# Optimization experiments

Measured on AMD Instinct MI355X. Metric: run time of the kernel, lower is better.

The kernel has to match this reference:

```python
import jax, jax.numpy as jnp
import numpy as np

N_HEAD = 16
D_K = 64


def _bn(x, g, b, eps=1e-5):
    # torch BatchNorm1d in training mode: biased batch variance
    m = jnp.mean(x, axis=0)
    v = jnp.var(x, axis=0)
    return (x - m) * jax.lax.rsqrt(v + eps) * g + b


def setup_inputs() -> dict:
    key = jax.random.key(0)
    ks = jax.random.split(key, 8)
    B, DX, NK, DKIN, H, DK, DO = 128, 1024, 1024, 512, N_HEAD, D_K, 512
    sc = 0.02
    return {
        "x": jax.random.normal(ks[0], (B, DX), dtype=jnp.float32),
        "k": jax.random.normal(ks[1], (B, NK, DKIN), dtype=jnp.float32),
        "bn1_g": jnp.ones((DX,), jnp.float32),
        "bn1_b": jnp.zeros((DX,), jnp.float32),
        "Wx": jax.random.normal(ks[2], (H * DK, DX), dtype=jnp.float32) * sc,
        "bx": jnp.zeros((H * DK,), jnp.float32),
        "Wk": jax.random.normal(ks[3], (H * DK, DKIN), dtype=jnp.float32) * sc,
        "bk": jnp.zeros((H * DK,), jnp.float32),
        "bn2_g": jnp.ones((DK,), jnp.float32),
        "bn2_b": jnp.zeros((DK,), jnp.float32),
        "Wlin": jax.random.normal(ks[4], (DK, DK), dtype=jnp.float32) * sc,
        "blin": jnp.zeros((DK,), jnp.float32),
        "Wo": jax.random.normal(ks[5], (DO, H * DK), dtype=jnp.float32) * sc,
        "bo": jnp.zeros((DO,), jnp.float32),
    }


def reference(x, k, bn1_g, bn1_b, Wx, bx, Wk, bk, bn2_g, bn2_b, Wlin, blin, Wo, bo):
    H, DK = N_HEAD, D_K
    B, DX = x.shape
    NK = k.shape[1]
    # outer BN + query projection (n_x == 1)
    xq = _bn(x, bn1_g, bn1_b) @ Wx.T + bx                     # (B, H*DK)
    xq = xq.reshape(B, H, DK).transpose(1, 0, 2).reshape(H * B, DK)
    kp = (k @ Wk.T + bk).reshape(B, NK, H, DK)
    kp = kp.transpose(2, 0, 1, 3).reshape(H * B, NK, DK)       # (H*B, NK, DK)
    # inner CrossAttention: BN + linear on the single query vector
    latent = _bn(xq, bn2_g, bn2_b) @ Wlin.T + blin             # (H*B, DK)
    u = jnp.einsum('bnd,bd->bn', kp, latent)                   # (H*B, NK)
    # softmax over the singleton query dim (dim=2) -> all ones, kept faithful
    attn = jax.nn.softmax(u[..., None], axis=-1)[..., 0]       # (H*B, NK)
    out = jnp.einsum('bnd,bn->bd', kp, attn)                   # (H*B, DK)
    out = out.reshape(H, B, DK).transpose(1, 0, 2).reshape(B, H * DK)
    x_hid = latent.reshape(H, B, DK).transpose(1, 0, 2).reshape(B, H * DK)
    # attn.view(n_head, batch, d_x_).permute(1,2,0).contiguous().view(batch, n_head, -1)
    attn_out = attn.reshape(H, B, NK).transpose(1, 2, 0).reshape(B, H, -1)
    return (attn_out, out @ Wo.T + bo, x_hid @ Wo.T + bo)
```

## Files before the change

### kernel.cpp

```cpp
#include <hip/hip_runtime.h>

typedef __attribute__((ext_vector_type(8))) short short8;
typedef __attribute__((ext_vector_type(4))) float floatx4;

__device__ __forceinline__ unsigned short f2bf(float f) {
    unsigned int x = __float_as_uint(f);
    x = x + 0x7FFFu + ((x >> 16) & 1u);
    return (unsigned short)(x >> 16);
}

__global__ __launch_bounds__(256) void k_reduce(
    const float* __restrict__ kk, float* __restrict__ part)
{
    int blk = blockIdx.x, tid = threadIdx.x;
    int b = blk >> 3, c = blk & 7;
    int f4 = tid & 127;
    int rh = tid >> 7;
    const float4* base = (const float4*)kk
        + ((size_t)(b * 1024 + c * 128 + rh) * 128 + f4);
    float4 acc = {0.f, 0.f, 0.f, 0.f};
    #pragma unroll 8
    for (int it = 0; it < 64; ++it) {
        float4 v = base[(size_t)it * 256];
        acc.x += v.x; acc.y += v.y; acc.z += v.z; acc.w += v.w;
    }
    __shared__ float red[2][512];
    red[rh][f4 * 4 + 0] = acc.x;
    red[rh][f4 * 4 + 1] = acc.y;
    red[rh][f4 * 4 + 2] = acc.z;
    red[rh][f4 * 4 + 3] = acc.w;
    __syncthreads();
    for (int j = tid; j < 512; j += 256)
        part[((size_t)(c * 128 + b) << 9) + j] = red[0][j] + red[1][j];
}

__global__ __launch_bounds__(256) void k_w2bf(
    const float* __restrict__ Wx, const float* __restrict__ Wk,
    const float* __restrict__ Wo, const float* __restrict__ Wl,
    unsigned short* __restrict__ Wxbf, unsigned short* __restrict__ Wkbf,
    unsigned short* __restrict__ Wobf, unsigned short* __restrict__ Wlbf)
{
    int f = blockIdx.x * 256 + threadIdx.x;
    const float* src; unsigned short* dst; int off;
    if (f < 262144)      { src = Wx; dst = Wxbf; off = f; }
    else if (f < 393216) { src = Wk; dst = Wkbf; off = f - 262144; }
    else if (f < 524288) { src = Wo; dst = Wobf; off = f - 393216; }
    else                 { src = Wl; dst = Wlbf; off = f - 524288; }
    float4 v = ((const float4*)src)[off];
    uint2 o;
    o.x = (unsigned int)f2bf(v.x) | ((unsigned int)f2bf(v.y) << 16);
    o.y = (unsigned int)f2bf(v.z) | ((unsigned int)f2bf(v.w) << 16);
    *(uint2*)(dst + off * 4) = o;
}

__global__ __launch_bounds__(256) void k_bn1_combine(
    const float* __restrict__ x, const float* __restrict__ g1,
    const float* __restrict__ b1, const float* __restrict__ part,
    unsigned short* __restrict__ xnbf, unsigned short* __restrict__ ksumbf)
{
    int blk = blockIdx.x, tid = threadIdx.x;
    if (blk < 4) {
        int c = blk * 256 + tid;
        float s = 0.f, ss = 0.f;
        #pragma unroll 8
        for (int b = 0; b < 128; ++b) {
            float v = x[b * 1024 + c];
            s += v; ss += v * v;
        }
        float m  = s * (1.f / 128.f);
        float va = ss * (1.f / 128.f) - m * m;
        float rs = rsqrtf(va + 1e-5f);
        float a  = rs * g1[c];
        float b2 = b1[c] - m * a;
        #pragma unroll 8
        for (int b = 0; b < 128; ++b)
            xnbf[b * 1024 + c] = f2bf(x[b * 1024 + c] * a + b2);
    } else {
        int idx = (blk - 4) * 256 + tid;
        int b = idx >> 6;
        int j0 = (idx & 63) * 8;
        float s[8];
        #pragma unroll
        for (int u = 0; u < 8; ++u) s[u] = 0.f;
        #pragma unroll
        for (int c = 0; c < 8; ++c) {
            const float4* p = (const float4*)(part + ((size_t)(c * 128 + b) << 9) + j0);
            float4 a0 = p[0], a1 = p[1];
            s[0] += a0.x; s[1] += a0.y; s[2] += a0.z; s[3] += a0.w;
            s[4] += a1.x; s[5] += a1.y; s[6] += a1.z; s[7] += a1.w;
        }
        uint4 v;
        v.x = (unsigned int)f2bf(s[0]) | ((unsigned int)f2bf(s[1]) << 16);
        v.y = (unsigned int)f2bf(s[2]) | ((unsigned int)f2bf(s[3]) << 16);
        v.z = (unsigned int)f2bf(s[4]) | ((unsigned int)f2bf(s[5]) << 16);
        v.w = (unsigned int)f2bf(s[6]) | ((unsigned int)f2bf(s[7]) << 16);
        *(uint4*)(ksumbf + b * 512 + j0) = v;
    }
}

template <typename OutT>
__global__ __launch_bounds__(256) void k_mfma(
    const unsigned short* __restrict__ A, int lda,
    const unsigned short* __restrict__ B, int ldb,
    const float* __restrict__ bias, float bscale,
    OutT* __restrict__ C, int ldc, int tilesN, int K)
{
    int gid = blockIdx.x * 256 + threadIdx.x;
    int wave = gid >> 6;
    int lane = threadIdx.x & 63;
    int tm = wave / tilesN, tn = wave % tilesN;
    int mn = lane & 15, q = lane >> 4;

    const short8* ap = (const short8*)(A + (size_t)(tm * 16 + mn) * lda + q * 8);
    const short8* bp = (const short8*)(B + (size_t)(tn * 16 + mn) * ldb + q * 8);

    floatx4 acc = {0.f, 0.f, 0.f, 0.f};
    #pragma unroll 4
    for (int k = 0; k < K; k += 32) {
        short8 a = *ap; ap += 4;
        short8 b = *bp; bp += 4;
        acc = __builtin_amdgcn_mfma_f32_16x16x32_bf16(a, b, acc, 0, 0, 0);
    }
    int col = tn * 16 + mn;
    float bv = bias[col] * bscale;
    #pragma unroll
    for (int r = 0; r < 4; ++r) {
        int row = tm * 16 + q * 4 + r;
        float v = acc[r] + bv;
        OutT* dst = C + (size_t)row * ldc + col;
        if constexpr (sizeof(OutT) == 2) *dst = (OutT)f2bf(v);
        else                             *dst = (OutT)v;
    }
}

__global__ __launch_bounds__(256) void k_bn2(
    const float* __restrict__ xq, const float* __restrict__ g2,
    const float* __restrict__ b2, float* __restrict__ ab)
{
    int d = blockIdx.x, tid = threadIdx.x;
    float s = 0.f, ss = 0.f;
    for (int e = tid; e < 2048; e += 256) {
        int b = e >> 4, h = e & 15;
        float v = xq[b * 1024 + h * 64 + d];
        s += v; ss += v * v;
    }
    __shared__ float r1[256], r2[256];
    r1[tid] = s; r2[tid] = ss;
    __syncthreads();
    for (int off = 128; off; off >>= 1) {
        if (tid < off) { r1[tid] += r1[tid + off]; r2[tid] += r2[tid + off]; }
        __syncthreads();
    }
    if (tid == 0) {
        float m  = r1[0] * (1.f / 2048.f);
        float va = r2[0] * (1.f / 2048.f) - m * m;
        float rs = rsqrtf(va + 1e-5f);
        float a  = rs * g2[d];
        ab[d] = a;
        ab[64 + d] = b2[d] - m * a;
    }
}

__global__ __launch_bounds__(256) void k_latent(
    const float* __restrict__ xq, const float* __restrict__ ab,
    const unsigned short* __restrict__ Wlbf, const float* __restrict__ bl,
    unsigned short* __restrict__ xhid)
{
    int tid = threadIdx.x;
    int r = tid >> 6, dp = tid & 63;
    int row = blockIdx.x * 4 + r;
    int h = row >> 7, b = row & 127;
    __shared__ float xs[4][64];
    xs[r][dp] = xq[b * 1024 + h * 64 + dp] * ab[dp] + ab[64 + dp];
    __syncthreads();
    float dot = bl[dp];
    #pragma unroll 16
    for (int d = 0; d < 64; ++d)
        dot += xs[r][d] * __uint_as_float(((unsigned int)Wlbf[dp * 64 + d]) << 16);
    xhid[b * 1024 + h * 64 + dp] = f2bf(dot);
}

__global__ __launch_bounds__(256) void k_ones(float4* __restrict__ attn_out)
{
    int idx = blockIdx.x * 256 + threadIdx.x;
    float4 ones = {1.f, 1.f, 1.f, 1.f};
    attn_out[idx] = ones;
}

extern "C" void kernel_launch(void* const* d_in, const int* in_sizes, int n_in,
                              void* d_out, int out_size, void* d_ws, size_t ws_size,
                              hipStream_t stream) {
    (void)d_ws; (void)ws_size; (void)in_sizes; (void)n_in; (void)out_size;
    const float* x  = (const float*)d_in[0];
    const float* kk = (const float*)d_in[1];
    const float* g1 = (const float*)d_in[2];
    const float* b1 = (const float*)d_in[3];
    const float* Wx = (const float*)d_in[4];
    const float* bx = (const float*)d_in[5];
    const float* Wk = (const float*)d_in[6];
    const float* bk = (const float*)d_in[7];
    const float* g2 = (const float*)d_in[8];
    const float* b2 = (const float*)d_in[9];
    const float* Wl = (const float*)d_in[10];
    const float* bl = (const float*)d_in[11];
    const float* Wo = (const float*)d_in[12];
    const float* bo = (const float*)d_in[13];

    char* ob = (char*)d_out;
    float*          part   = (float*)(ob + 0);
    unsigned short* Wxbf   = (unsigned short*)(ob + 2097152);
    unsigned short* Wkbf   = (unsigned short*)(ob + 4194304);
    unsigned short* Wobf   = (unsigned short*)(ob + 5242880);
    unsigned short* Wlbf   = (unsigned short*)(ob + 6291456);
    unsigned short* xnbf   = (unsigned short*)(ob + 6299648);
    unsigned short* ksumbf = (unsigned short*)(ob + 6561792);
    float*          xq     = (float*)(ob + 6692864);
    float*          ab     = (float*)(ob + 7217152);
    unsigned short* concat = (unsigned short*)(ob + 7217664);
    float*          out12  = (float*)d_out + 2097152;

    k_reduce<<<1024, 256, 0, stream>>>(kk, part);
    k_w2bf<<<2052, 256, 0, stream>>>(Wx, Wk, Wo, Wl, Wxbf, Wkbf, Wobf, Wlbf);
    k_bn1_combine<<<36, 256, 0, stream>>>(x, g1, b1, part, xnbf, ksumbf);
    k_mfma<float><<<128, 256, 0, stream>>>(xnbf, 1024, Wxbf, 1024, bx, 1.f, xq, 1024, 64, 1024);
    k_mfma<unsigned short><<<128, 256, 0, stream>>>(ksumbf, 512, Wkbf, 512, bk, 1024.f, concat, 1024, 64, 512);
    k_bn2<<<64, 256, 0, stream>>>(xq, g2, b2, ab);
    k_latent<<<512, 256, 0, stream>>>(xq, ab, Wlbf, bl, concat + 131072);
    k_mfma<float><<<128, 256, 0, stream>>>(concat, 1024, Wobf, 1024, bo, 1.f, out12, 512, 32, 1024);
    k_ones<<<2048, 256, 0, stream>>>((float4*)d_out);
}
```

Before: 446.2 us.

## Merge independent stages into fewer launches and move scratch buffers to workspace

Combines the k reduction, weight bf16 conversion, ones fill and BN1 normalization into one heterogeneous-block kernel. The two projection GEMMs are merged into one launch, and the ksum combine is split out into its own kernel. Scratch buffers move from the output buffer to the workspace, which lets the ones fill run early without being overwritten. The aim is to cut launch count and serialization gaps between small independent kernels. The cost is one extra launch for the split-out combine, and the BN1 blocks now run as the last blocks of a large grid.

```diff
diff --git a/kernel.cpp b/kernel.cpp
--- a/kernel.cpp
+++ b/kernel.cpp
@@ -9,58 +9,85 @@
     return (unsigned short)(x >> 16);
 }
 
-__global__ __launch_bounds__(256) void k_reduce(
-    const float* __restrict__ kk, float* __restrict__ part)
-{
-    int blk = blockIdx.x, tid = threadIdx.x;
-    int b = blk >> 3, c = blk & 7;
-    int f4 = tid & 127;
-    int rh = tid >> 7;
-    const float4* base = (const float4*)kk
-        + ((size_t)(b * 1024 + c * 128 + rh) * 128 + f4);
-    float4 acc = {0.f, 0.f, 0.f, 0.f};
-    #pragma unroll 8
-    for (int it = 0; it < 64; ++it) {
-        float4 v = base[(size_t)it * 256];
-        acc.x += v.x; acc.y += v.y; acc.z += v.z; acc.w += v.w;
-    }
-    __shared__ float red[2][512];
-    red[rh][f4 * 4 + 0] = acc.x;
-    red[rh][f4 * 4 + 1] = acc.y;
-    red[rh][f4 * 4 + 2] = acc.z;
-    red[rh][f4 * 4 + 3] = acc.w;
-    __syncthreads();
-    for (int j = tid; j < 512; j += 256)
-        part[((size_t)(c * 128 + b) << 9) + j] = red[0][j] + red[1][j];
-}
-
-__global__ __launch_bounds__(256) void k_w2bf(
+template <typename OutT>
+__device__ __forceinline__ void gemm_tile(
+    const unsigned short* __restrict__ A, int lda,
+    const unsigned short* __restrict__ B, int ldb,
+    const float* __restrict__ bias, float bscale,
+    OutT* __restrict__ C, int ldc, int tilesN, int K, int wave, int lane)
+{
+    int tm = wave / tilesN, tn = wave % tilesN;
+    int mn = lane & 15, q = lane >> 4;
+    const short8* ap = (const short8*)(A + (size_t)(tm * 16 + mn) * lda + q * 8);
+    const short8* bp = (const short8*)(B + (size_t)(tn * 16 + mn) * ldb + q * 8);
+    floatx4 acc = {0.f, 0.f, 0.f, 0.f};
+    #pragma unroll 4
+    for (int k = 0; k < K; k += 32) {
+        short8 a = *ap; ap += 4;
+        short8 b = *bp; bp += 4;
+        acc = __builtin_amdgcn_mfma_f32_16x16x32_bf16(a, b, acc, 0, 0, 0);
+    }
+    int col = tn * 16 + mn;
+    float bv = bias[col] * bscale;
+    #pragma unroll
+    for (int r = 0; r < 4; ++r) {
+        int row = tm * 16 + q * 4 + r;
+        float v = acc[r] + bv;
+        OutT* dst = C + (size_t)row * ldc + col;
+        if constexpr (sizeof(OutT) == 2) *dst = (OutT)f2bf(v);
+        else                             *dst = (OutT)v;
+    }
+}
+
+__global__ __launch_bounds__(256) void k_mega(
+    const float* __restrict__ kk, float* __restrict__ part,
     const float* __restrict__ Wx, const float* __restrict__ Wk,
     const float* __restrict__ Wo, const float* __restrict__ Wl,
     unsigned short* __restrict__ Wxbf, unsigned short* __restrict__ Wkbf,
-    unsigned short* __restrict__ Wobf, unsigned short* __restrict__ Wlbf)
-{
-    int f = blockIdx.x * 256 + threadIdx.x;
-    const float* src; unsigned short* dst; int off;
-    if (f < 262144)      { src = Wx; dst = Wxbf; off = f; }
-    else if (f < 393216) { src = Wk; dst = Wkbf; off = f - 262144; }
-    else if (f < 524288) { src = Wo; dst = Wobf; off = f - 393216; }
-    else                 { src = Wl; dst = Wlbf; off = f - 524288; }
-    float4 v = ((const float4*)src)[off];
-    uint2 o;
-    o.x = (unsigned int)f2bf(v.x) | ((unsigned int)f2bf(v.y) << 16);
-    o.y = (unsigned int)f2bf(v.z) | ((unsigned int)f2bf(v.w) << 16);
-    *(uint2*)(dst + off * 4) = o;
-}
-
-__global__ __launch_bounds__(256) void k_bn1_combine(
+    unsigned short* __restrict__ Wobf, unsigned short* __restrict__ Wlbf,
+    float4* __restrict__ attn_out,
     const float* __restrict__ x, const float* __restrict__ g1,
-    const float* __restrict__ b1, const float* __restrict__ part,
-    unsigned short* __restrict__ xnbf, unsigned short* __restrict__ ksumbf)
+    const float* __restrict__ b1, unsigned short* __restrict__ xnbf)
 {
     int blk = blockIdx.x, tid = threadIdx.x;
-    if (blk < 4) {
-        int c = blk * 256 + tid;
+    if (blk < 1024) {
+        int b = blk >> 3, c = blk & 7;
+        int f4 = tid & 127;
+        int rh = tid >> 7;
+        const float4* base = (const float4*)kk
+            + ((size_t)(b * 1024 + c * 128 + rh) * 128 + f4);
+        float4 acc = {0.f, 0.f, 0.f, 0.f};
+        #pragma unroll 8
+        for (int it = 0; it < 64; ++it) {
+            float4 v = base[(size_t)it * 256];
+            acc.x += v.x; acc.y += v.y; acc.z += v.z; acc.w += v.w;
+        }
+        __shared__ float red[2][512];
+        red[rh][f4 * 4 + 0] = acc.x;
+        red[rh][f4 * 4 + 1] = acc.y;
+        red[rh][f4 * 4 + 2] = acc.z;
+        red[rh][f4 * 4 + 3] = acc.w;
+        __syncthreads();
+        for (int j = tid; j < 512; j += 256)
+            part[((size_t)(c * 128 + b) << 9) + j] = red[0][j] + red[1][j];
+    } else if (blk < 3076) {
+        int f = (blk - 1024) * 256 + tid;
+        const float* src; unsigned short* dst; int off;
+        if (f < 262144)      { src = Wx; dst = Wxbf; off = f; }
+        else if (f < 393216) { src = Wk; dst = Wkbf; off = f - 262144; }
+        else if (f < 524288) { src = Wo; dst = Wobf; off = f - 393216; }
+        else                 { src = Wl; dst = Wlbf; off = f - 524288; }
+        float4 v = ((const float4*)src)[off];
+        uint2 o;
+        o.x = (unsigned int)f2bf(v.x) | ((unsigned int)f2bf(v.y) << 16);
+        o.y = (unsigned int)f2bf(v.z) | ((unsigned int)f2bf(v.w) << 16);
+        *(uint2*)(dst + off * 4) = o;
+    } else if (blk < 5124) {
+        int idx = (blk - 3076) * 256 + tid;
+        float4 ones = {1.f, 1.f, 1.f, 1.f};
+        attn_out[idx] = ones;
+    } else {
+        int c = (blk - 5124) * 256 + tid;
         float s = 0.f, ss = 0.f;
         #pragma unroll 8
         for (int b = 0; b < 128; ++b) {
@@ -75,61 +102,46 @@
         #pragma unroll 8
         for (int b = 0; b < 128; ++b)
             xnbf[b * 1024 + c] = f2bf(x[b * 1024 + c] * a + b2);
+    }
+}
+
+__global__ __launch_bounds__(256) void k_combine(
+    const float* __restrict__ part, unsigned short* __restrict__ ksumbf)
+{
+    int idx = blockIdx.x * 256 + threadIdx.x;
+    int b = idx >> 6;
+    int j0 = (idx & 63) * 8;
+    float s[8];
+    #pragma unroll
+    for (int u = 0; u < 8; ++u) s[u] = 0.f;
+    #pragma unroll
+    for (int c = 0; c < 8; ++c) {
+        const float4* p = (const float4*)(part + ((size_t)(c * 128 + b) << 9) + j0);
+        float4 a0 = p[0], a1 = p[1];
+        s[0] += a0.x; s[1] += a0.y; s[2] += a0.z; s[3] += a0.w;
+        s[4] += a1.x; s[5] += a1.y; s[6] += a1.z; s[7] += a1.w;
+    }
+    uint4 v;
+    v.x = (unsigned int)f2bf(s[0]) | ((unsigned int)f2bf(s[1]) << 16);
+    v.y = (unsigned int)f2bf(s[2]) | ((unsigned int)f2bf(s[3]) << 16);
+    v.z = (unsigned int)f2bf(s[4]) | ((unsigned int)f2bf(s[5]) << 16);
+    v.w = (unsigned int)f2bf(s[6]) | ((unsigned int)f2bf(s[7]) << 16);
+    *(uint4*)(ksumbf + b * 512 + j0) = v;
+}
+
+__global__ __launch_bounds__(256) void k_dual_gemm(
+    const unsigned short* __restrict__ xnbf, const unsigned short* __restrict__ Wxbf,
+    const float* __restrict__ bx, float* __restrict__ xq,
+    const unsigned short* __restrict__ ksumbf, const unsigned short* __restrict__ Wkbf,
+    const float* __restrict__ bk, unsigned short* __restrict__ concat)
+{
+    int blk = blockIdx.x, tid = threadIdx.x, lane = tid & 63;
+    if (blk < 128) {
+        int wave = (blk * 256 + tid) >> 6;
+        gemm_tile<float>(xnbf, 1024, Wxbf, 1024, bx, 1.f, xq, 1024, 64, 1024, wave, lane);
     } else {
-        int idx = (blk - 4) * 256 + tid;
-        int b = idx >> 6;
-        int j0 = (idx & 63) * 8;
-        float s[8];
-        #pragma unroll
-        for (int u = 0; u < 8; ++u) s[u] = 0.f;
-        #pragma unroll
-        for (int c = 0; c < 8; ++c) {
-            const float4* p = (const float4*)(part + ((size_t)(c * 128 + b) << 9) + j0);
-            float4 a0 = p[0], a1 = p[1];
-            s[0] += a0.x; s[1] += a0.y; s[2] += a0.z; s[3] += a0.w;
-            s[4] += a1.x; s[5] += a1.y; s[6] += a1.z; s[7] += a1.w;
-        }
-        uint4 v;
-        v.x = (unsigned int)f2bf(s[0]) | ((unsigned int)f2bf(s[1]) << 16);
-        v.y = (unsigned int)f2bf(s[2]) | ((unsigned int)f2bf(s[3]) << 16);
-        v.z = (unsigned int)f2bf(s[4]) | ((unsigned int)f2bf(s[5]) << 16);
-        v.w = (unsigned int)f2bf(s[6]) | ((unsigned int)f2bf(s[7]) << 16);
-        *(uint4*)(ksumbf + b * 512 + j0) = v;
-    }
-}
-
-template <typename OutT>
-__global__ __launch_bounds__(256) void k_mfma(
-    const unsigned short* __restrict__ A, int lda,
-    const unsigned short* __restrict__ B, int ldb,
-    const float* __restrict__ bias, float bscale,
-    OutT* __restrict__ C, int ldc, int tilesN, int K)
-{
-    int gid = blockIdx.x * 256 + threadIdx.x;
-    int wave = gid >> 6;
-    int lane = threadIdx.x & 63;
-    int tm = wave / tilesN, tn = wave % tilesN;
-    int mn = lane & 15, q = lane >> 4;
-
-    const short8* ap = (const short8*)(A + (size_t)(tm * 16 + mn) * lda + q * 8);
-    const short8* bp = (const short8*)(B + (size_t)(tn * 16 + mn) * ldb + q * 8);
-
-    floatx4 acc = {0.f, 0.f, 0.f, 0.f};
-    #pragma unroll 4
-    for (int k = 0; k < K; k += 32) {
-        short8 a = *ap; ap += 4;
-        short8 b = *bp; bp += 4;
-        acc = __builtin_amdgcn_mfma_f32_16x16x32_bf16(a, b, acc, 0, 0, 0);
-    }
-    int col = tn * 16 + mn;
-    float bv = bias[col] * bscale;
-    #pragma unroll
-    for (int r = 0; r < 4; ++r) {
-        int row = tm * 16 + q * 4 + r;
-        float v = acc[r] + bv;
-        OutT* dst = C + (size_t)row * ldc + col;
-        if constexpr (sizeof(OutT) == 2) *dst = (OutT)f2bf(v);
-        else                             *dst = (OutT)v;
+        int wave = ((blk - 128) * 256 + tid) >> 6;
+        gemm_tile<unsigned short>(ksumbf, 512, Wkbf, 512, bk, 1024.f, concat, 1024, 64, 512, wave, lane);
     }
 }
 
@@ -180,17 +192,19 @@
     xhid[b * 1024 + h * 64 + dp] = f2bf(dot);
 }
 
-__global__ __launch_bounds__(256) void k_ones(float4* __restrict__ attn_out)
-{
-    int idx = blockIdx.x * 256 + threadIdx.x;
-    float4 ones = {1.f, 1.f, 1.f, 1.f};
-    attn_out[idx] = ones;
+__global__ __launch_bounds__(256) void k_final_gemm(
+    const unsigned short* __restrict__ concat, const unsigned short* __restrict__ Wobf,
+    const float* __restrict__ bo, float* __restrict__ out12)
+{
+    int wave = (blockIdx.x * 256 + threadIdx.x) >> 6;
+    gemm_tile<float>(concat, 1024, Wobf, 1024, bo, 1.f, out12, 512, 32, 1024,
+                     wave, threadIdx.x & 63);
 }
 
 extern "C" void kernel_launch(void* const* d_in, const int* in_sizes, int n_in,
                               void* d_out, int out_size, void* d_ws, size_t ws_size,
                               hipStream_t stream) {
-    (void)d_ws; (void)ws_size; (void)in_sizes; (void)n_in; (void)out_size;
+    (void)in_sizes; (void)n_in; (void)out_size; (void)ws_size;
     const float* x  = (const float*)d_in[0];
     const float* kk = (const float*)d_in[1];
     const float* g1 = (const float*)d_in[2];
@@ -206,26 +220,25 @@
     const float* Wo = (const float*)d_in[12];
     const float* bo = (const float*)d_in[13];
 
-    char* ob = (char*)d_out;
-    float*          part   = (float*)(ob + 0);
-    unsigned short* Wxbf   = (unsigned short*)(ob + 2097152);
-    unsigned short* Wkbf   = (unsigned short*)(ob + 4194304);
-    unsigned short* Wobf   = (unsigned short*)(ob + 5242880);
-    unsigned short* Wlbf   = (unsigned short*)(ob + 6291456);
-    unsigned short* xnbf   = (unsigned short*)(ob + 6299648);
-    unsigned short* ksumbf = (unsigned short*)(ob + 6561792);
-    float*          xq     = (float*)(ob + 6692864);
-    float*          ab     = (float*)(ob + 7217152);
-    unsigned short* concat = (unsigned short*)(ob + 7217664);
+    char* ws = (char*)d_ws;
+    float*          part   = (float*)(ws + 0);
+    unsigned short* Wxbf   = (unsigned short*)(ws + 2097152);
+    unsigned short* Wkbf   = (unsigned short*)(ws + 4194304);
+    unsigned short* Wobf   = (unsigned short*)(ws + 5242880);
+    unsigned short* Wlbf   = (unsigned short*)(ws + 6291456);
+    unsigned short* xnbf   = (unsigned short*)(ws + 6299648);
+    unsigned short* ksumbf = (unsigned short*)(ws + 6561792);
+    float*          xq     = (float*)(ws + 6692864);
+    float*          ab     = (float*)(ws + 7217152);
+    unsigned short* concat = (unsigned short*)(ws + 7217664);
     float*          out12  = (float*)d_out + 2097152;
 
-    k_reduce<<<1024, 256, 0, stream>>>(kk, part);
-    k_w2bf<<<2052, 256, 0, stream>>>(Wx, Wk, Wo, Wl, Wxbf, Wkbf, Wobf, Wlbf);
-    k_bn1_combine<<<36, 256, 0, stream>>>(x, g1, b1, part, xnbf, ksumbf);
-    k_mfma<float><<<128, 256, 0, stream>>>(xnbf, 1024, Wxbf, 1024, bx, 1.f, xq, 1024, 64, 1024);
-    k_mfma<unsigned short><<<128, 256, 0, stream>>>(ksumbf, 512, Wkbf, 512, bk, 1024.f, concat, 1024, 64, 512);
+    k_mega<<<5128, 256, 0, stream>>>(kk, part, Wx, Wk, Wo, Wl,
+                                     Wxbf, Wkbf, Wobf, Wlbf,
+                                     (float4*)d_out, x, g1, b1, xnbf);
+    k_combine<<<32, 256, 0, stream>>>(part, ksumbf);
+    k_dual_gemm<<<256, 256, 0, stream>>>(xnbf, Wxbf, bx, xq, ksumbf, Wkbf, bk, concat);
     k_bn2<<<64, 256, 0, stream>>>(xq, g2, b2, ab);
     k_latent<<<512, 256, 0, stream>>>(xq, ab, Wlbf, bl, concat + 131072);
-    k_mfma<float><<<128, 256, 0, stream>>>(concat, 1024, Wobf, 1024, bo, 1.f, out12, 512, 32, 1024);
-    k_ones<<<2048, 256, 0, stream>>>((float4*)d_out);
-}
+    k_final_gemm<<<128, 256, 0, stream>>>(concat, Wobf, bo, out12);
+}
```

After: 427.4 us. 1.04x faster.
